# Kernel optimization log

Hardware: AMD Instinct MI355X
Metric: run time of the kernel (lower is better)

Reference implementation:

```python
import jax, jax.numpy as jnp
import numpy as np

B, T, D, H = 1, 4096, 1024, 16
HD = D // H  # 64
ROPE_BASE = 10000.0


def rotate_half(x):
    x1, x2 = jnp.split(x, 2, axis=-1)
    return jnp.concatenate([-x2, x1], axis=-1)


def rope_sin_cos(t, head_dim, dtype):
    inv_freq = 1.0 / (ROPE_BASE ** (jnp.arange(0, head_dim, 2, dtype=jnp.float32) / head_dim))
    pos = jnp.arange(t, dtype=jnp.float32)
    freqs = pos[:, None] * inv_freq[None, :]          # [T, HD/2]
    emb = jnp.concatenate([freqs, freqs], axis=-1)    # [T, HD]
    return jnp.sin(emb).astype(dtype), jnp.cos(emb).astype(dtype)


def setup_inputs() -> dict:
    key = jax.random.key(0)
    kx, kq, kp = jax.random.split(key, 3)
    scale = 0.02
    x = jax.random.normal(kx, (B, T, D), dtype=jnp.float32)
    W_qkv = jax.random.normal(kq, (3 * D, D), dtype=jnp.float32) * scale  # torch Linear weight [out,in]
    W_proj = jax.random.normal(kp, (D, D), dtype=jnp.float32) * scale
    return {"x": x, "W_qkv": W_qkv, "W_proj": W_proj}


def reference(x, W_qkv, W_proj):
    b, t, d = x.shape
    qkv = jnp.einsum('btd,ed->bte', x, W_qkv)                 # [B,T,3D]
    qkv = qkv.reshape(b, t, 3, H, HD)
    q, k, v = (qkv[:, :, i].transpose(0, 2, 1, 3) for i in range(3))  # each [B,H,T,HD]
    sin, cos = rope_sin_cos(t, HD, x.dtype)                    # [T,HD]
    q = q * cos + rotate_half(q) * sin
    k = k * cos + rotate_half(k) * sin
    scores = jnp.einsum('bhqd,bhkd->bhqk', q, k) / jnp.sqrt(jnp.asarray(HD, x.dtype))
    mask = jnp.triu(jnp.full((t, t), -jnp.inf, dtype=x.dtype), k=1)
    attn = jax.nn.softmax(scores + mask, axis=-1)
    out = jnp.einsum('bhqk,bhkd->bhqd', attn, v)               # [B,H,T,HD]
    out = out.transpose(0, 2, 1, 3).reshape(b, t, d)
    return jnp.einsum('btd,ed->bte', out, W_proj)
```

## Files before the change

kernel.cpp:

```cpp
#include <hip/hip_runtime.h>
#include <hip/hip_bf16.h>
#include <stdint.h>

#define TSEQ 4096
#define DM   1024
#define NH   16
#define HD   64
#define NQKV 3072

typedef unsigned short u16;
typedef unsigned int   u32;
typedef __attribute__((ext_vector_type(8)))  short bf16x8;
typedef __attribute__((ext_vector_type(4)))  float f32x4;
typedef __attribute__((ext_vector_type(16))) float f32x16;
typedef __attribute__((ext_vector_type(4)))  int   i32x4;

static __device__ __forceinline__ u16 f2bf(float f) {
  u32 u = __float_as_uint(f);
  u32 r = (u + 0x7FFFu + ((u >> 16) & 1u)) >> 16;
  return (u16)r;
}
static __device__ __forceinline__ float bf2f(u16 u) {
  return __uint_as_float(((u32)u) << 16);
}
static __device__ __forceinline__ u32 cvt_pk_bf16(float lo, float hi) {
  u32 r;
  asm("v_cvt_pk_bf16_f32 %0, %1, %2" : "=v"(r) : "v"(lo), "v"(hi));
  return r;
}
static __device__ __forceinline__ float fexp2(float x) {
  float r;
  asm("v_exp_f32 %0, %1" : "=v"(r) : "v"(x));
  return r;
}

#define GLL16(g, l) __builtin_amdgcn_global_load_lds( \
    (const __attribute__((address_space(1))) u32*)(g), \
    (__attribute__((address_space(3))) u32*)(l), 16, 0, 0)

#define N4X  (TSEQ * DM / 4)
#define N4Q  (NQKV * DM / 4)
#define N4P  (DM * DM / 4)
__global__ void cast3_kernel(const float* __restrict__ x, u16* __restrict__ xo,
                             const float* __restrict__ wq, u16* __restrict__ wqo,
                             const float* __restrict__ wp, u16* __restrict__ wpo) {
  int i = blockIdx.x * 256 + threadIdx.x;
  const float* in; u16* out; int k;
  if (i < N4X)            { in = x;  out = xo;  k = i; }
  else if (i < N4X + N4Q) { in = wq; out = wqo; k = i - N4X; }
  else if (i < N4X + N4Q + N4P) { in = wp; out = wpo; k = i - N4X - N4Q; }
  else return;
  float4 v = ((const float4*)in)[k];
  ushort4 o;
  o.x = f2bf(v.x); o.y = f2bf(v.y); o.z = f2bf(v.z); o.w = f2bf(v.w);
  ((ushort4*)out)[k] = o;
}

__global__ void rope_table(float* __restrict__ sT, float* __restrict__ cT) {
  int i = blockIdx.x * 256 + threadIdx.x;
  int t = i >> 5, j = i & 31;
  float inv = exp2f((float)j * (-13.287712379549449f / 32.0f));
  float ang = (float)t * inv;
  sT[i] = sinf(ang);
  cT[i] = cosf(ang);
}

__global__ __launch_bounds__(512) void gemm_qkv(const u16* __restrict__ A,
                                                const u16* __restrict__ B,
                                                const float* __restrict__ sT,
                                                const float* __restrict__ cT,
                                                u16* __restrict__ Qo,
                                                u16* __restrict__ Ko,
                                                u16* __restrict__ Vo)
{
  const int K = DM;
  __shared__ __align__(16) u16 As[2][128 * 32];
  __shared__ __align__(16) u16 Bs[2][128 * 32];
  const int tid  = threadIdx.x;
  const int wave = tid >> 6, lane = tid & 63;
  const int l15  = lane & 15, lh = lane >> 4;
  const int wr   = wave >> 1, wc = wave & 1;

  int lin = blockIdx.y * gridDim.x + blockIdx.x;
  const int xcd = lin & 7, idx = lin >> 3;
  const size_t bm = (size_t)((xcd & 3) * 8 + idx / 12);
  const size_t bn = (size_t)((xcd >> 2) * 12 + idx % 12);

  f32x4 acc[2][4] = {};

  const u16* Ab = A + bm * 128 * (size_t)K;
  const u16* Bb = B + bn * 128 * (size_t)K;

  const int ea = tid * 8, ra = ea >> 5;
  const int cs = (((tid & 3) ^ (ra & 3)) << 3);
  const int xo = ((lh ^ (l15 & 3)) << 3);

  GLL16(Ab + (size_t)ra * K + cs, &As[0][ea]);
  GLL16(Bb + (size_t)ra * K + cs, &Bs[0][ea]);
  asm volatile("s_waitcnt vmcnt(0)" ::: "memory");
  __syncthreads();

  int cur = 0;
  for (int k0 = 0; k0 < K; k0 += 32, cur ^= 1) {
    if (k0 + 32 < K) {
      const int kn = k0 + 32;
      GLL16(Ab + (size_t)ra * K + kn + cs, &As[cur ^ 1][ea]);
      GLL16(Bb + (size_t)ra * K + kn + cs, &Bs[cur ^ 1][ea]);
    }

    bf16x8 af[2], bfr[4];
#pragma unroll
    for (int m = 0; m < 2; ++m)
      af[m] = *(const bf16x8*)(&As[cur][(wr * 32 + m * 16 + l15) * 32 + xo]);
#pragma unroll
    for (int n = 0; n < 4; ++n)
      bfr[n] = *(const bf16x8*)(&Bs[cur][(wc * 64 + n * 16 + l15) * 32 + xo]);
    __builtin_amdgcn_s_setprio(1);
#pragma unroll
    for (int m = 0; m < 2; ++m)
#pragma unroll
      for (int n = 0; n < 4; ++n)
        acc[m][n] = __builtin_amdgcn_mfma_f32_16x16x32_bf16(af[m], bfr[n], acc[m][n], 0, 0, 0);
    __builtin_amdgcn_s_setprio(0);

    asm volatile("s_waitcnt vmcnt(0)" ::: "memory");
    __syncthreads();
  }

  const float QSC = 0.125f * 1.4426950408889634f;
  const int gcb = (int)(bn * 128) + wc * 64;
  const int rg  = gcb >> 10;
  const int hh2 = (gcb >> 6) & 15;
  const size_t hb = (size_t)hh2 * 128;

  if (rg < 2) {
    u16* dst = rg ? Ko : Qo;
    const float sc = rg ? 1.f : QSC;
#pragma unroll
    for (int m = 0; m < 2; ++m)
#pragma unroll
      for (int r = 0; r < 4; ++r) {
        int t = (int)(bm * 128) + wr * 32 + m * 16 + lh * 4 + r;
        size_t tb = (hb + (t >> 5)) * 2048 + (size_t)(t & 31) * 8;
#pragma unroll
        for (int n = 0; n < 2; ++n) {
          int d  = n * 16 + l15;
          int d2 = d + 32;
          float s = sT[t * 32 + d], c = cT[t * 32 + d];
          float v1 = acc[m][n][r], v2 = acc[m][n + 2][r];
          dst[tb + (d  >> 4) * 512 + ((d  >> 3) & 1) * 256 + (d  & 7)] =
              f2bf((v1 * c - v2 * s) * sc);
          dst[tb + (d2 >> 4) * 512 + ((d2 >> 3) & 1) * 256 + (d2 & 7)] =
              f2bf((v2 * c + v1 * s) * sc);
        }
      }
  } else {
#pragma unroll
    for (int m = 0; m < 2; ++m)
#pragma unroll
      for (int r = 0; r < 4; ++r) {
        int t = (int)(bm * 128) + wr * 32 + m * 16 + lh * 4 + r;
        size_t tb = (hb + (t >> 5)) * 2048 + (size_t)((t >> 4) & 1) * 512 +
                    ((t >> 3) & 1) * 256 + (t & 7);
#pragma unroll
        for (int n = 0; n < 4; ++n) {
          int d = n * 16 + l15;
          Vo[tb + (size_t)(d >> 5) * 1024 + (size_t)(d & 31) * 8] = f2bf(acc[m][n][r]);
        }
      }
  }
}

__global__ __launch_bounds__(256) void gemm_proj(const u16* __restrict__ A,
                                                 const u16* __restrict__ B,
                                                 float* __restrict__ Cout,
                                                 int M, int N, int K)
{
  __shared__ __align__(16) u16 As[2][64 * 32];
  __shared__ __align__(16) u16 Bs[2][64 * 32];
  const int tid  = threadIdx.x;
  const int wave = tid >> 6, lane = tid & 63;
  const int l15  = lane & 15, lh = lane >> 4;
  const int wr   = wave >> 1, wc = wave & 1;

  int lin = blockIdx.y * gridDim.x + blockIdx.x;
  const int xcd = lin & 7, idx = lin >> 3;
  const size_t bm = (size_t)((xcd & 3) * 16 + idx / 8);
  const size_t bn = (size_t)((xcd >> 2) * 8 + idx % 8);

  f32x4 acc[2][2] = {};

  const u16* Ab = A + bm * 64 * (size_t)K;
  const u16* Bb = B + bn * 64 * (size_t)K;

  const int ea = wave * 512 + lane * 8, ra = ea >> 5;
  const int cs = (((lane & 3) ^ (ra & 3)) << 3);
  const int xo = ((lh ^ (l15 & 3)) << 3);

  GLL16(Ab + (size_t)ra * K + cs, &As[0][wave * 512]);
  GLL16(Bb + (size_t)ra * K + cs, &Bs[0][wave * 512]);
  asm volatile("s_waitcnt vmcnt(0)" ::: "memory");
  __syncthreads();

  int cur = 0;
  for (int k0 = 0; k0 < K; k0 += 32, cur ^= 1) {
    if (k0 + 32 < K) {
      const int kn = k0 + 32;
      GLL16(Ab + (size_t)ra * K + kn + cs, &As[cur ^ 1][wave * 512]);
      GLL16(Bb + (size_t)ra * K + kn + cs, &Bs[cur ^ 1][wave * 512]);
    }

    bf16x8 af[2], bfr[2];
#pragma unroll
    for (int m = 0; m < 2; ++m)
      af[m] = *(const bf16x8*)(&As[cur][(wr * 32 + m * 16 + l15) * 32 + xo]);
#pragma unroll
    for (int n = 0; n < 2; ++n)
      bfr[n] = *(const bf16x8*)(&Bs[cur][(wc * 32 + n * 16 + l15) * 32 + xo]);
    __builtin_amdgcn_s_setprio(1);
#pragma unroll
    for (int m = 0; m < 2; ++m)
#pragma unroll
      for (int n = 0; n < 2; ++n)
        acc[m][n] = __builtin_amdgcn_mfma_f32_16x16x32_bf16(af[m], bfr[n], acc[m][n], 0, 0, 0);
    __builtin_amdgcn_s_setprio(0);

    asm volatile("s_waitcnt vmcnt(0)" ::: "memory");
    __syncthreads();
  }

#pragma unroll
  for (int m = 0; m < 2; ++m)
#pragma unroll
    for (int n = 0; n < 2; ++n)
#pragma unroll
      for (int r = 0; r < 4; ++r) {
        size_t row = bm * 64 + wr * 32 + m * 16 + lh * 4 + r;
        size_t col = bn * 64 + wc * 32 + n * 16 + l15;
        Cout[row * N + col] = acc[m][n][r];
      }
}

__global__ __launch_bounds__(256, 4) void fattn(const u16* __restrict__ Qf,
                                                const u16* __restrict__ Kf,
                                                const u16* __restrict__ Vf,
                                                u16* __restrict__ Op0,
                                                u16* __restrict__ Op123,
                                                float2* __restrict__ lmb)
{
  __shared__ __align__(16) u16 smem[8192];

  const int bid = blockIdx.x;
  const int h   = bid & (NH - 1);
  const int g   = (bid >> 4) & 3;
  const int qt  = 31 - (bid >> 6);
  const int tid = threadIdx.x;
  const int wave = tid >> 6, lane = tid & 63;
  const int l31 = lane & 31, hh = lane >> 5;
  const int lb  = lane * 8;

  const size_t hbase = (size_t)h * (TSEQ * HD);
  const u16* kg = Kf + hbase;
  const u16* vg = Vf + hbase;
  u16* const Og = g ? (Op123 + (size_t)(g - 1) * (TSEQ * DM)) : Op0;

  const int q0  = qt * 128;
  const int per = qt + 1;
  const int kt0 = g * per, kt1 = kt0 + per;
  const int qw0 = q0 + wave * 32;
  const int qgl = qw0 + l31;

  f32x16 oacc0 = {}, oacc1 = {};
  float mrun = 0.f, lrunp = 0.f;

  bf16x8 qf[4];
  {
    const u16* qp = Qf + hbase + (size_t)(qt * 4 + wave) * 2048;
#pragma unroll
    for (int kc = 0; kc < 4; ++kc)
      qf[kc] = *(const bf16x8*)(qp + kc * 512 + lb);
  }

  GLL16(kg + (size_t)kt0 * 2048 + tid * 8, smem + tid * 8);
  GLL16(vg + (size_t)kt0 * 2048 + tid * 8, smem + 4096 + tid * 8);
  asm volatile("s_waitcnt vmcnt(0)" ::: "memory");
  __syncthreads();

  for (int kt = kt0; kt < kt1; ++kt) {
    const int cur = (kt - kt0) & 1;
    if (kt + 1 < kt1) {
      GLL16(kg + (size_t)(kt + 1) * 2048 + tid * 8, smem + (cur ^ 1) * 2048 + tid * 8);
      GLL16(vg + (size_t)(kt + 1) * 2048 + tid * 8, smem + 4096 + (cur ^ 1) * 2048 + tid * 8);
    }
    const u16* kb = smem + cur * 2048;
    const u16* vb = smem + 4096 + cur * 2048;
    const int kv0 = kt * 32;

    const float mz = (kt == kt0) ? 0.f : -mrun;
    f32x16 s0;
    __builtin_amdgcn_s_setprio(1);
    {
      f32x16 z;
#pragma unroll
      for (int i2 = 0; i2 < 16; ++i2) z[i2] = mz;
      bf16x8 kf0 = *(const bf16x8*)(kb + lb);
      s0 = __builtin_amdgcn_mfma_f32_32x32x16_bf16(kf0, qf[0], z, 0, 0, 0);
    }
#pragma unroll
    for (int kc = 1; kc < 4; ++kc) {
      bf16x8 kf = *(const bf16x8*)(kb + kc * 512 + lb);
      s0 = __builtin_amdgcn_mfma_f32_32x32x16_bf16(kf, qf[kc], s0, 0, 0, 0);
    }
    __builtin_amdgcn_s_setprio(0);

    if (kv0 + 31 > qw0) {
#pragma unroll
      for (int r = 0; r < 16; ++r) {
        int kvr = kv0 + (r & 3) + 8 * (r >> 2) + 4 * hh;
        if (kvr > qgl) s0[r] = -3.0e38f;
      }
    }

    if (kt == kt0) {
      float tm = -3.0e38f;
#pragma unroll
      for (int r = 0; r < 16; ++r) tm = fmaxf(tm, s0[r]);
      tm = fmaxf(tm, __shfl_xor(tm, 32));
      mrun = tm;
#pragma unroll
      for (int r = 0; r < 16; ++r) s0[r] -= mrun;
    }

    float rs = 0.f;
#pragma unroll
    for (int r = 0; r < 16; ++r) {
      s0[r] = fexp2(s0[r]);
      rs += s0[r];
    }
    lrunp += rs;

    bf16x8 pf[2];
#pragma unroll
    for (int kc = 0; kc < 2; ++kc) {
      const int e = 8 * kc;
      u32 Xa = cvt_pk_bf16(s0[e + 0], s0[e + 1]);
      u32 Xb = cvt_pk_bf16(s0[e + 2], s0[e + 3]);
      u32 Ya = cvt_pk_bf16(s0[e + 4], s0[e + 5]);
      u32 Yb = cvt_pk_bf16(s0[e + 6], s0[e + 7]);
      asm volatile("v_permlane32_swap_b32 %0, %1" : "+v"(Xa), "+v"(Ya));
      asm volatile("v_permlane32_swap_b32 %0, %1" : "+v"(Xb), "+v"(Yb));
      union { u32 u[4]; bf16x8 v; } pu;
      pu.u[0] = Xa; pu.u[1] = Xb; pu.u[2] = Ya; pu.u[3] = Yb;
      pf[kc] = pu.v;
    }

    __builtin_amdgcn_s_setprio(1);
#pragma unroll
    for (int s2 = 0; s2 < 2; ++s2) {
      bf16x8 v0 = *(const bf16x8*)(vb + (0 * 2 + s2) * 512 + lb);
      bf16x8 v1 = *(const bf16x8*)(vb + (1 * 2 + s2) * 512 + lb);
      oacc0 = __builtin_amdgcn_mfma_f32_32x32x16_bf16(v0, pf[s2], oacc0, 0, 0, 0);
      oacc1 = __builtin_amdgcn_mfma_f32_32x32x16_bf16(v1, pf[s2], oacc1, 0, 0, 0);
    }
    __builtin_amdgcn_s_setprio(0);

    asm volatile("s_waitcnt vmcnt(0)" ::: "memory");
    __syncthreads();
  }

  {
    float lr = lrunp + __shfl_xor(lrunp, 32);
    float inv = 1.f / lr;
    u16* scr = smem + wave * 2048;
#pragma unroll
    for (int dt = 0; dt < 2; ++dt)
#pragma unroll
      for (int rq = 0; rq < 4; ++rq) {
        float v0 = (dt ? oacc1[4 * rq + 0] : oacc0[4 * rq + 0]) * inv;
        float v1 = (dt ? oacc1[4 * rq + 1] : oacc0[4 * rq + 1]) * inv;
        float v2 = (dt ? oacc1[4 * rq + 2] : oacc0[4 * rq + 2]) * inv;
        float v3 = (dt ? oacc1[4 * rq + 3] : oacc0[4 * rq + 3]) * inv;
        uint2 wv;
        wv.x = cvt_pk_bf16(v0, v1);
        wv.y = cvt_pk_bf16(v2, v3);
        int g2 = 4 * dt + rq;
        *(uint2*)(scr + l31 * 64 + ((g2 ^ (l31 & 7)) * 8) + 4 * hh) = wv;
      }
    asm volatile("s_waitcnt lgkmcnt(0)" ::: "memory");
    __builtin_amdgcn_sched_barrier(0);
    const int q  = lane >> 1;
    const int dh = lane & 1;
#pragma unroll
    for (int c2 = 0; c2 < 4; ++c2) {
      int gg = dh * 4 + c2;
      i32x4 v = *(const i32x4*)(scr + q * 64 + ((gg ^ (q & 7)) * 8));
      *(i32x4*)(Og + (size_t)(qw0 + q) * DM + h * HD + dh * 32 + c2 * 8) = v;
    }
    if (hh == 0)
      lmb[((size_t)g * NH + h) * TSEQ + qgl] = make_float2(mrun, lr);
  }
}

__global__ void merge_o(const u16* __restrict__ Op0, const u16* __restrict__ Op123,
                        const float2* __restrict__ lmb, u16* __restrict__ Ob) {
  int i = blockIdx.x * 256 + threadIdx.x;
  int q  = i >> 7;
  int c8 = (i & 127) * 8;
  int h  = c8 >> 6;
  float2 s0 = lmb[(size_t)h * TSEQ + q];
  float2 s1 = lmb[((size_t)NH + h) * TSEQ + q];
  float2 s2 = lmb[((size_t)2 * NH + h) * TSEQ + q];
  float2 s3 = lmb[((size_t)3 * NH + h) * TSEQ + q];
  float m  = fmaxf(fmaxf(s0.x, s1.x), fmaxf(s2.x, s3.x));
  float w0 = fexp2(s0.x - m) * s0.y;
  float w1 = fexp2(s1.x - m) * s1.y;
  float w2 = fexp2(s2.x - m) * s2.y;
  float w3 = fexp2(s3.x - m) * s3.y;
  float inv = 1.f / (w0 + w1 + w2 + w3);
  float a0 = w0 * inv, a1 = w1 * inv, a2 = w2 * inv, a3 = w3 * inv;
  size_t off = (size_t)q * DM + c8;
  i32x4 u0 = *(const i32x4*)(Op0 + off);
  i32x4 u1 = *(const i32x4*)(Op123 + off);
  i32x4 u2 = *(const i32x4*)(Op123 + (size_t)(TSEQ * DM) + off);
  i32x4 u3 = *(const i32x4*)(Op123 + 2 * (size_t)(TSEQ * DM) + off);
  const u16* p0 = (const u16*)&u0;
  const u16* p1 = (const u16*)&u1;
  const u16* p2 = (const u16*)&u2;
  const u16* p3 = (const u16*)&u3;
  union { u16 o[8]; i32x4 v; } r;
#pragma unroll
  for (int e = 0; e < 8; ++e)
    r.o[e] = f2bf(a0 * bf2f(p0[e]) + a1 * bf2f(p1[e]) +
                  a2 * bf2f(p2[e]) + a3 * bf2f(p3[e]));
  *(i32x4*)(Ob + off) = r.v;
}

extern "C" void kernel_launch(void* const* d_in, const int* in_sizes, int n_in,
                              void* d_out, int out_size, void* d_ws, size_t ws_size,
                              hipStream_t stream)
{
  const float* x     = (const float*)d_in[0];
  const float* wqkv  = (const float*)d_in[1];
  const float* wproj = (const float*)d_in[2];
  float* out = (float*)d_out;

  char* ws = (char*)d_ws;
  size_t off = 0;
  u16* xb   = (u16*)(ws + off); off += (size_t)TSEQ * DM * 2;
  u16* wqb  = (u16*)(ws + off); off += (size_t)NQKV * DM * 2;
  u16* wpb  = (u16*)(ws + off); off += (size_t)DM * DM * 2;
  u16* qkvb = (u16*)(ws + off); off += (size_t)TSEQ * NQKV * 2;
  u16* Qb   = (u16*)(ws + off); off += (size_t)NH * TSEQ * HD * 2;
  u16* Kb   = (u16*)(ws + off); off += (size_t)NH * TSEQ * HD * 2;
  u16* Vb   = (u16*)(ws + off); off += (size_t)NH * TSEQ * HD * 2;
  u16* Ob   = (u16*)(ws + off); off += (size_t)TSEQ * DM * 2;
  float* sT = (float*)(ws + off); off += (size_t)TSEQ * 32 * 4;
  float* cT = (float*)(ws + off); off += (size_t)TSEQ * 32 * 4;

  u16*    Op123 = qkvb;
  float2* lmb   = (float2*)wqb;

  const int ncast = N4X + N4Q + N4P;
  cast3_kernel<<<(ncast + 255) / 256, 256, 0, stream>>>(x, xb, wqkv, wqb, wproj, wpb);
  rope_table<<<(TSEQ * 32) / 256, 256, 0, stream>>>(sT, cT);

  gemm_qkv<<<dim3(NQKV / 128, TSEQ / 128), 512, 0, stream>>>(xb, wqb, sT, cT, Qb, Kb, Vb);

  fattn<<<NH * 32 * 4, 256, 0, stream>>>(Qb, Kb, Vb, Ob, Op123, lmb);

  merge_o<<<(TSEQ * DM / 8) / 256, 256, 0, stream>>>(Ob, Op123, lmb, Ob);

  gemm_proj<<<dim3(DM / 64, TSEQ / 64), 256, 0, stream>>>(Ob, wpb, out, TSEQ, DM, DM);
}
```

Baseline: 123.4 us.

## Double KV tile size to 64 keys and rebalance split-K ranges

```diff
diff --git a/kernel.cpp b/kernel.cpp
--- a/kernel.cpp
+++ b/kernel.cpp
@@ -248,7 +248,7 @@
                                                 u16* __restrict__ Op123,
                                                 float2* __restrict__ lmb)
 {
-  __shared__ __align__(16) u16 smem[8192];
+  __shared__ __align__(16) u16 smem[16384];
 
   const int bid = blockIdx.x;
   const int h   = bid & (NH - 1);
@@ -265,13 +265,14 @@
   u16* const Og = g ? (Op123 + (size_t)(g - 1) * (TSEQ * DM)) : Op0;
 
   const int q0  = qt * 128;
-  const int per = qt + 1;
-  const int kt0 = g * per, kt1 = kt0 + per;
+  const int ntiles = 2 * (qt + 1);
+  const int kt0 = (g * ntiles) >> 2;
+  const int kt1 = ((g + 1) * ntiles) >> 2;
   const int qw0 = q0 + wave * 32;
   const int qgl = qw0 + l31;
 
   f32x16 oacc0 = {}, oacc1 = {};
-  float mrun = 0.f, lrunp = 0.f;
+  float mrun = -3.0e38f, lrunp = 0.f;
 
   bf16x8 qf[4];
   {
@@ -281,120 +282,154 @@
       qf[kc] = *(const bf16x8*)(qp + kc * 512 + lb);
   }
 
-  GLL16(kg + (size_t)kt0 * 2048 + tid * 8, smem + tid * 8);
-  GLL16(vg + (size_t)kt0 * 2048 + tid * 8, smem + 4096 + tid * 8);
-  asm volatile("s_waitcnt vmcnt(0)" ::: "memory");
-  __syncthreads();
-
-  for (int kt = kt0; kt < kt1; ++kt) {
-    const int cur = (kt - kt0) & 1;
-    if (kt + 1 < kt1) {
-      GLL16(kg + (size_t)(kt + 1) * 2048 + tid * 8, smem + (cur ^ 1) * 2048 + tid * 8);
-      GLL16(vg + (size_t)(kt + 1) * 2048 + tid * 8, smem + 4096 + (cur ^ 1) * 2048 + tid * 8);
-    }
-    const u16* kb = smem + cur * 2048;
-    const u16* vb = smem + 4096 + cur * 2048;
-    const int kv0 = kt * 32;
-
-    const float mz = (kt == kt0) ? 0.f : -mrun;
-    f32x16 s0;
-    __builtin_amdgcn_s_setprio(1);
-    {
-      f32x16 z;
-#pragma unroll
-      for (int i2 = 0; i2 < 16; ++i2) z[i2] = mz;
-      bf16x8 kf0 = *(const bf16x8*)(kb + lb);
-      s0 = __builtin_amdgcn_mfma_f32_32x32x16_bf16(kf0, qf[0], z, 0, 0, 0);
-    }
-#pragma unroll
-    for (int kc = 1; kc < 4; ++kc) {
-      bf16x8 kf = *(const bf16x8*)(kb + kc * 512 + lb);
-      s0 = __builtin_amdgcn_mfma_f32_32x32x16_bf16(kf, qf[kc], s0, 0, 0, 0);
-    }
-    __builtin_amdgcn_s_setprio(0);
-
-    if (kv0 + 31 > qw0) {
-#pragma unroll
-      for (int r = 0; r < 16; ++r) {
-        int kvr = kv0 + (r & 3) + 8 * (r >> 2) + 4 * hh;
-        if (kvr > qgl) s0[r] = -3.0e38f;
-      }
-    }
-
-    if (kt == kt0) {
-      float tm = -3.0e38f;
-#pragma unroll
-      for (int r = 0; r < 16; ++r) tm = fmaxf(tm, s0[r]);
-      tm = fmaxf(tm, __shfl_xor(tm, 32));
-      mrun = tm;
-#pragma unroll
-      for (int r = 0; r < 16; ++r) s0[r] -= mrun;
-    }
-
-    float rs = 0.f;
-#pragma unroll
-    for (int r = 0; r < 16; ++r) {
-      s0[r] = fexp2(s0[r]);
-      rs += s0[r];
-    }
-    lrunp += rs;
-
-    bf16x8 pf[2];
-#pragma unroll
-    for (int kc = 0; kc < 2; ++kc) {
-      const int e = 8 * kc;
-      u32 Xa = cvt_pk_bf16(s0[e + 0], s0[e + 1]);
-      u32 Xb = cvt_pk_bf16(s0[e + 2], s0[e + 3]);
-      u32 Ya = cvt_pk_bf16(s0[e + 4], s0[e + 5]);
-      u32 Yb = cvt_pk_bf16(s0[e + 6], s0[e + 7]);
-      asm volatile("v_permlane32_swap_b32 %0, %1" : "+v"(Xa), "+v"(Ya));
-      asm volatile("v_permlane32_swap_b32 %0, %1" : "+v"(Xb), "+v"(Yb));
-      union { u32 u[4]; bf16x8 v; } pu;
-      pu.u[0] = Xa; pu.u[1] = Xb; pu.u[2] = Ya; pu.u[3] = Yb;
-      pf[kc] = pu.v;
-    }
-
-    __builtin_amdgcn_s_setprio(1);
-#pragma unroll
-    for (int s2 = 0; s2 < 2; ++s2) {
-      bf16x8 v0 = *(const bf16x8*)(vb + (0 * 2 + s2) * 512 + lb);
-      bf16x8 v1 = *(const bf16x8*)(vb + (1 * 2 + s2) * 512 + lb);
-      oacc0 = __builtin_amdgcn_mfma_f32_32x32x16_bf16(v0, pf[s2], oacc0, 0, 0, 0);
-      oacc1 = __builtin_amdgcn_mfma_f32_32x32x16_bf16(v1, pf[s2], oacc1, 0, 0, 0);
-    }
-    __builtin_amdgcn_s_setprio(0);
-
+  if (kt0 < kt1) {
+    GLL16(kg + (size_t)kt0 * 4096 + tid * 8,        smem + tid * 8);
+    GLL16(kg + (size_t)kt0 * 4096 + 2048 + tid * 8, smem + 2048 + tid * 8);
+    GLL16(vg + (size_t)kt0 * 4096 + tid * 8,        smem + 8192 + tid * 8);
+    GLL16(vg + (size_t)kt0 * 4096 + 2048 + tid * 8, smem + 8192 + 2048 + tid * 8);
     asm volatile("s_waitcnt vmcnt(0)" ::: "memory");
     __syncthreads();
+
+    for (int kt = kt0; kt < kt1; ++kt) {
+      const int cur = (kt - kt0) & 1;
+      if (kt + 1 < kt1) {
+        const size_t nb = (size_t)(kt + 1) * 4096;
+        u16* kd = smem + (cur ^ 1) * 4096;
+        u16* vd = smem + 8192 + (cur ^ 1) * 4096;
+        GLL16(kg + nb + tid * 8,        kd + tid * 8);
+        GLL16(kg + nb + 2048 + tid * 8, kd + 2048 + tid * 8);
+        GLL16(vg + nb + tid * 8,        vd + tid * 8);
+        GLL16(vg + nb + 2048 + tid * 8, vd + 2048 + tid * 8);
+      }
+      const u16* kb = smem + cur * 4096;
+      const u16* vb = smem + 8192 + cur * 4096;
+      const int kv0 = kt * 64;
+
+      const float mz = (kt == kt0) ? 0.f : -mrun;
+      f32x16 s0, s1;
+      __builtin_amdgcn_s_setprio(1);
+      {
+        f32x16 z;
+#pragma unroll
+        for (int i2 = 0; i2 < 16; ++i2) z[i2] = mz;
+        bf16x8 ka = *(const bf16x8*)(kb + lb);
+        bf16x8 kbf = *(const bf16x8*)(kb + 2048 + lb);
+        s0 = __builtin_amdgcn_mfma_f32_32x32x16_bf16(ka,  qf[0], z, 0, 0, 0);
+        s1 = __builtin_amdgcn_mfma_f32_32x32x16_bf16(kbf, qf[0], z, 0, 0, 0);
+      }
+#pragma unroll
+      for (int kc = 1; kc < 4; ++kc) {
+        bf16x8 ka = *(const bf16x8*)(kb + kc * 512 + lb);
+        bf16x8 kbf = *(const bf16x8*)(kb + 2048 + kc * 512 + lb);
+        s0 = __builtin_amdgcn_mfma_f32_32x32x16_bf16(ka,  qf[kc], s0, 0, 0, 0);
+        s1 = __builtin_amdgcn_mfma_f32_32x32x16_bf16(kbf, qf[kc], s1, 0, 0, 0);
+      }
+      __builtin_amdgcn_s_setprio(0);
+
+      if (kv0 + 63 > qw0) {
+#pragma unroll
+        for (int r = 0; r < 16; ++r) {
+          int kvr = kv0 + (r & 3) + 8 * (r >> 2) + 4 * hh;
+          if (kvr > qgl)      s0[r] = -3.0e38f;
+          if (kvr + 32 > qgl) s1[r] = -3.0e38f;
+        }
+      }
+
+      if (kt == kt0) {
+        float tm = -3.0e38f;
+#pragma unroll
+        for (int r = 0; r < 16; ++r) tm = fmaxf(fmaxf(tm, s0[r]), s1[r]);
+        tm = fmaxf(tm, __shfl_xor(tm, 32));
+        mrun = tm;
+#pragma unroll
+        for (int r = 0; r < 16; ++r) { s0[r] -= mrun; s1[r] -= mrun; }
+      }
+
+      float rs = 0.f;
+#pragma unroll
+      for (int r = 0; r < 16; ++r) {
+        s0[r] = fexp2(s0[r]);
+        s1[r] = fexp2(s1[r]);
+        rs += s0[r] + s1[r];
+      }
+      lrunp += rs;
+
+      bf16x8 pf[4];
+#pragma unroll
+      for (int kc = 0; kc < 2; ++kc) {
+        const int e = 8 * kc;
+        u32 Xa = cvt_pk_bf16(s0[e + 0], s0[e + 1]);
+        u32 Xb = cvt_pk_bf16(s0[e + 2], s0[e + 3]);
+        u32 Ya = cvt_pk_bf16(s0[e + 4], s0[e + 5]);
+        u32 Yb = cvt_pk_bf16(s0[e + 6], s0[e + 7]);
+        asm volatile("v_permlane32_swap_b32 %0, %1" : "+v"(Xa), "+v"(Ya));
+        asm volatile("v_permlane32_swap_b32 %0, %1" : "+v"(Xb), "+v"(Yb));
+        union { u32 u[4]; bf16x8 v; } pu;
+        pu.u[0] = Xa; pu.u[1] = Xb; pu.u[2] = Ya; pu.u[3] = Yb;
+        pf[kc] = pu.v;
+      }
+#pragma unroll
+      for (int kc = 0; kc < 2; ++kc) {
+        const int e = 8 * kc;
+        u32 Xa = cvt_pk_bf16(s1[e + 0], s1[e + 1]);
+        u32 Xb = cvt_pk_bf16(s1[e + 2], s1[e + 3]);
+        u32 Ya = cvt_pk_bf16(s1[e + 4], s1[e + 5]);
+        u32 Yb = cvt_pk_bf16(s1[e + 6], s1[e + 7]);
+        asm volatile("v_permlane32_swap_b32 %0, %1" : "+v"(Xa), "+v"(Ya));
+        asm volatile("v_permlane32_swap_b32 %0, %1" : "+v"(Xb), "+v"(Yb));
+        union { u32 u[4]; bf16x8 v; } pu;
+        pu.u[0] = Xa; pu.u[1] = Xb; pu.u[2] = Ya; pu.u[3] = Yb;
+        pf[2 + kc] = pu.v;
+      }
+
+      __builtin_amdgcn_s_setprio(1);
+#pragma unroll
+      for (int s2 = 0; s2 < 2; ++s2) {
+        bf16x8 v00 = *(const bf16x8*)(vb + s2 * 512 + lb);
+        bf16x8 v10 = *(const bf16x8*)(vb + 1024 + s2 * 512 + lb);
+        oacc0 = __builtin_amdgcn_mfma_f32_32x32x16_bf16(v00, pf[s2], oacc0, 0, 0, 0);
+        oacc1 = __builtin_amdgcn_mfma_f32_32x32x16_bf16(v10, pf[s2], oacc1, 0, 0, 0);
+        bf16x8 v01 = *(const bf16x8*)(vb + 2048 + s2 * 512 + lb);
+        bf16x8 v11 = *(const bf16x8*)(vb + 3072 + s2 * 512 + lb);
+        oacc0 = __builtin_amdgcn_mfma_f32_32x32x16_bf16(v01, pf[2 + s2], oacc0, 0, 0, 0);
+        oacc1 = __builtin_amdgcn_mfma_f32_32x32x16_bf16(v11, pf[2 + s2], oacc1, 0, 0, 0);
+      }
+      __builtin_amdgcn_s_setprio(0);
+
+      asm volatile("s_waitcnt vmcnt(0)" ::: "memory");
+      __syncthreads();
+    }
   }
 
   {
     float lr = lrunp + __shfl_xor(lrunp, 32);
-    float inv = 1.f / lr;
-    u16* scr = smem + wave * 2048;
-#pragma unroll
-    for (int dt = 0; dt < 2; ++dt)
-#pragma unroll
-      for (int rq = 0; rq < 4; ++rq) {
-        float v0 = (dt ? oacc1[4 * rq + 0] : oacc0[4 * rq + 0]) * inv;
-        float v1 = (dt ? oacc1[4 * rq + 1] : oacc0[4 * rq + 1]) * inv;
-        float v2 = (dt ? oacc1[4 * rq + 2] : oacc0[4 * rq + 2]) * inv;
-        float v3 = (dt ? oacc1[4 * rq + 3] : oacc0[4 * rq + 3]) * inv;
-        uint2 wv;
-        wv.x = cvt_pk_bf16(v0, v1);
-        wv.y = cvt_pk_bf16(v2, v3);
-        int g2 = 4 * dt + rq;
-        *(uint2*)(scr + l31 * 64 + ((g2 ^ (l31 & 7)) * 8) + 4 * hh) = wv;
-      }
-    asm volatile("s_waitcnt lgkmcnt(0)" ::: "memory");
-    __builtin_amdgcn_sched_barrier(0);
-    const int q  = lane >> 1;
-    const int dh = lane & 1;
-#pragma unroll
-    for (int c2 = 0; c2 < 4; ++c2) {
-      int gg = dh * 4 + c2;
-      i32x4 v = *(const i32x4*)(scr + q * 64 + ((gg ^ (q & 7)) * 8));
-      *(i32x4*)(Og + (size_t)(qw0 + q) * DM + h * HD + dh * 32 + c2 * 8) = v;
+    if (kt0 < kt1) {
+      float inv = 1.f / lr;
+      u16* scr = smem + wave * 2048;
+#pragma unroll
+      for (int dt = 0; dt < 2; ++dt)
+#pragma unroll
+        for (int rq = 0; rq < 4; ++rq) {
+          float v0 = (dt ? oacc1[4 * rq + 0] : oacc0[4 * rq + 0]) * inv;
+          float v1 = (dt ? oacc1[4 * rq + 1] : oacc0[4 * rq + 1]) * inv;
+          float v2 = (dt ? oacc1[4 * rq + 2] : oacc0[4 * rq + 2]) * inv;
+          float v3 = (dt ? oacc1[4 * rq + 3] : oacc0[4 * rq + 3]) * inv;
+          uint2 wv;
+          wv.x = cvt_pk_bf16(v0, v1);
+          wv.y = cvt_pk_bf16(v2, v3);
+          int g2 = 4 * dt + rq;
+          *(uint2*)(scr + l31 * 64 + ((g2 ^ (l31 & 7)) * 8) + 4 * hh) = wv;
+        }
+      asm volatile("s_waitcnt lgkmcnt(0)" ::: "memory");
+      __builtin_amdgcn_sched_barrier(0);
+      const int q  = lane >> 1;
+      const int dh = lane & 1;
+#pragma unroll
+      for (int c2 = 0; c2 < 4; ++c2) {
+        int gg = dh * 4 + c2;
+        i32x4 v = *(const i32x4*)(scr + q * 64 + ((gg ^ (q & 7)) * 8));
+        *(i32x4*)(Og + (size_t)(qw0 + q) * DM + h * HD + dh * 32 + c2 * 8) = v;
+      }
     }
     if (hh == 0)
       lmb[((size_t)g * NH + h) * TSEQ + qgl] = make_float2(mrun, lr);
```

After: 125.3 us. About the same (+1.5%).
